# Kernel optimization log

Hardware: AMD Instinct MI355X
Metric: run time of the kernel (lower is better)

Reference implementation:

```python
import jax, jax.numpy as jnp
import numpy as np

N = 32768   # points
C = 64      # channels (in == out, required by residual)
K = 16      # nsample
SP = 8      # share_planes
S = C // SP # attention channels per group
E = N * K


def _bn(t, g, b, eps=1e-5):
    # torch BatchNorm1d training-mode forward: biased batch variance
    m = t.mean(0)
    v = t.var(0)
    return (t - m) * jax.lax.rsqrt(v + eps) * g + b


def setup_inputs() -> dict:
    rng = np.random.default_rng(0)
    pos = (rng.standard_normal((N, 3)) * 10.0).astype(np.float32)
    # kNN graph (loop=True -> self is among the K nearest, distance 0), chunked
    sq = (pos ** 2).sum(1)
    nbr = np.empty((N, K), dtype=np.int64)
    chunk = 2048
    for s0 in range(0, N, chunk):
        s1 = min(s0 + chunk, N)
        d = sq[s0:s1, None] + sq[None, :] - 2.0 * (pos[s0:s1] @ pos.T)
        nbr[s0:s1] = np.argpartition(d, K - 1, axis=1)[:, :K]
    # PyG convention: edge_index[0]=source j (neighbor), edge_index[1]=target i
    edge_index = np.stack([nbr.reshape(-1),
                           np.repeat(np.arange(N, dtype=np.int64), K)])

    def lin_w(fo, fi):
        b = 1.0 / np.sqrt(fi)
        return jnp.asarray(rng.uniform(-b, b, size=(fo, fi)).astype(np.float32))

    def lin_b(fo, fi):
        b = 1.0 / np.sqrt(fi)
        return jnp.asarray(rng.uniform(-b, b, size=(fo,)).astype(np.float32))

    ones = lambda n: jnp.ones((n,), jnp.float32)
    zeros = lambda n: jnp.zeros((n,), jnp.float32)

    return {
        'pos': jnp.asarray(pos),
        'x': jnp.asarray(rng.standard_normal((N, C)).astype(np.float32)),
        'W1': lin_w(C, C),
        'Wk': lin_w(C, C), 'bk': lin_b(C, C),
        'Wq': lin_w(C, C), 'bq': lin_b(C, C),
        'Wv': lin_w(C, C), 'bv': lin_b(C, C),
        'p1_w': lin_w(3, 3), 'p1_b': lin_b(3, 3),
        'p_bn_g': ones(3), 'p_bn_b': zeros(3),
        'p2_w': lin_w(C, 3), 'p2_b': lin_b(C, 3),
        'w_bn1_g': ones(C), 'w_bn1_b': zeros(C),
        'w1_w': lin_w(S, C), 'w1_b': lin_b(S, C),
        'w_bn2_g': ones(S), 'w_bn2_b': zeros(S),
        'w2_w': lin_w(S, S), 'w2_b': lin_b(S, S),
        'W3': lin_w(C, C),
        'bn1_g': ones(C), 'bn1_b': zeros(C),
        'bn2_g': ones(C), 'bn2_b': zeros(C),
        'bn3_g': ones(C), 'bn3_b': zeros(C),
        'edge_index': jnp.asarray(edge_index),
    }


def reference(pos, x, W1, Wk, bk, Wq, bq, Wv, bv,
              p1_w, p1_b, p_bn_g, p_bn_b, p2_w, p2_b,
              w_bn1_g, w_bn1_b, w1_w, w1_b, w_bn2_g, w_bn2_b, w2_w, w2_b,
              W3, bn1_g, bn1_b, bn2_g, bn2_b, bn3_g, bn3_b, edge_index):
    x_skip = x
    h = jax.nn.relu(_bn(x @ W1.T, bn1_g, bn1_b))            # linear1 (no bias) + bn1 + relu

    # PointTransformerLayer
    k = h @ Wk.T + bk                                        # alpha_j source
    q = h @ Wq.T + bq                                        # alpha_i target
    v = h @ Wv.T + bv                                        # values
    src, dst = edge_index[0], edge_index[1]

    rel = pos[src] - pos[dst]                                # pos_j - pos_i  [E,3]
    delta = jax.nn.relu(_bn(rel @ p1_w.T + p1_b, p_bn_g, p_bn_b)) @ p2_w.T + p2_b  # [E,C]

    a = k[src] - q[dst] + delta                              # [E,C]
    a = jax.nn.relu(_bn(a, w_bn1_g, w_bn1_b)) @ w1_w.T + w1_b        # [E,S]
    a = jax.nn.relu(_bn(a, w_bn2_g, w_bn2_b)) @ w2_w.T + w2_b        # [E,S]

    # segment softmax over each target's neighborhood
    amax = jax.ops.segment_max(a, dst, num_segments=N)
    ae = jnp.exp(a - amax[dst])
    asum = jax.ops.segment_sum(ae, dst, num_segments=N)
    attn = ae / asum[dst]                                    # [E,S]

    # grouped weighted values: attn broadcast across the SP groups
    msg = (attn[:, None, :] * (v[src] + delta).reshape(E, SP, S)).reshape(E, C)
    out = jax.ops.segment_sum(msg, dst, num_segments=N)      # aggr='add' -> [N,C]

    h2 = jax.nn.relu(_bn(out, bn2_g, bn2_b))
    h3 = _bn(h2 @ W3.T, bn3_g, bn3_b)                        # linear3 (no bias) + bn3
    return jax.nn.relu(h3 + x_skip)
```

## Files before the change

kernel.cpp:

```cpp
#include <hip/hip_runtime.h>

#define NPTS 32768
#define CH 64
#define KNN 16
#define NE (NPTS*KNN)
#define EPS 1e-5f
#define NREP 32

#define G_P   0
#define G_BN1 (1*NREP*128)
#define G_W1  (2*NREP*128)
#define G_W2  (3*NREP*128)
#define G_BN2 (4*NREP*128)
#define G_BN3 (5*NREP*128)
#define STATS_FLOATS (6*NREP*128)

#define F_P   (STATS_FLOATS + 0*128)
#define F_BN1 (STATS_FLOATS + 1*128)
#define F_W1  (STATS_FLOATS + 2*128)
#define F_W2  (STATS_FLOATS + 3*128)
#define F_BN2 (STATS_FLOATS + 4*128)
#define F_BN3 (STATS_FLOATS + 5*128)

#define OFF_T1  (STATS_FLOATS + 1024)
#define SZ_NC   (NPTS*CH)
#define OFF_K   (OFF_T1 + SZ_NC)
#define OFF_Q   (OFF_K + NPTS*32)
#define OFF_V   (OFF_Q + NPTS*32)
#define OFF_A2  (OFF_V + NPTS*32)
#define OFF_OUT (OFF_A2 + NE*4)
#define OFF_U   (OFF_OUT + SZ_NC)
#define OFF_H3  OFF_U

typedef unsigned int uint;

__device__ __forceinline__ float frelu(float x){ return fmaxf(x, 0.f); }
__device__ __forceinline__ float bflo(uint u){ return __uint_as_float(u<<16); }
__device__ __forceinline__ float bfhi(uint u){ return __uint_as_float(u & 0xffff0000u); }
__device__ __forceinline__ uint bfpack(float lo, float hi){
    uint a = __float_as_uint(lo), b = __float_as_uint(hi);
    a = (a + 0x7fffu + ((a>>16)&1u)) >> 16;
    b = ((b + 0x7fffu + ((b>>16)&1u)) >> 16) << 16;
    return a | b;
}

__global__ __launch_bounds__(128) void k_fin(
    const float* __restrict__ gA, float invA, const float* __restrict__ gmA,
    const float* __restrict__ btA, float* __restrict__ outA, int nchA,
    const float* __restrict__ gB, float invB, const float* __restrict__ gmB,
    const float* __restrict__ btB, float* __restrict__ outB, int nchB)
{
    __shared__ float s_tmp[128];
    const int tid = threadIdx.x;
    const float* g; float inv; const float* gm; const float* bt; float* o; int nch;
    if (blockIdx.x == 0) { g=gA; inv=invA; gm=gmA; bt=btA; o=outA; nch=nchA; }
    else { if (!outB) return; g=gB; inv=invB; gm=gmB; bt=btB; o=outB; nch=nchB; }
    float t = 0.f;
    #pragma unroll
    for (int r=0;r<NREP;++r) t += g[r*128+tid];
    s_tmp[tid] = t;
    __syncthreads();
    if (tid < 64) {
        if (tid < nch) {
            float m = s_tmp[tid]*inv;
            float v = s_tmp[64+tid]*inv - m*m;
            float s = gm[tid]*rsqrtf(v+EPS);
            o[tid] = s; o[64+tid] = bt[tid] - m*s;
        } else { o[tid]=0.f; o[64+tid]=0.f; }
    }
}

__global__ __launch_bounds__(256) void k_pstats_u(
    const float* __restrict__ pos, const int* __restrict__ esrc,
    const float* __restrict__ p1w, const float* __restrict__ p1b,
    float4* __restrict__ u4, float* __restrict__ gstat)
{
    __shared__ float red[4][6];
    const int tid = threadIdx.x;
    const float w0=p1w[0],w1=p1w[1],w2=p1w[2],w3=p1w[3],w4=p1w[4],w5=p1w[5],w6=p1w[6],w7=p1w[7],w8=p1w[8];
    const float b0=p1b[0],b1=p1b[1],b2=p1b[2];
    const int e = blockIdx.x*256 + tid;
    const int sj = esrc[e]; const int d = e >> 4;
    float ax = pos[3*sj]-pos[3*d], ay = pos[3*sj+1]-pos[3*d+1], az = pos[3*sj+2]-pos[3*d+2];
    float u0 = w0*ax+w1*ay+w2*az+b0;
    float u1 = w3*ax+w4*ay+w5*az+b1;
    float u2 = w6*ax+w7*ay+w8*az+b2;
    u4[e] = make_float4(u0,u1,u2,0.f);
    float s0=u0,s1=u1,s2=u2,q0=u0*u0,q1=u1*u1,q2=u2*u2;
    #pragma unroll
    for (int m=32;m>=1;m>>=1){
        s0+=__shfl_xor(s0,m); s1+=__shfl_xor(s1,m); s2+=__shfl_xor(s2,m);
        q0+=__shfl_xor(q0,m); q1+=__shfl_xor(q1,m); q2+=__shfl_xor(q2,m);
    }
    const int wv = tid>>6;
    if ((tid&63)==0){ red[wv][0]=s0; red[wv][1]=s1; red[wv][2]=s2;
                      red[wv][3]=q0; red[wv][4]=q1; red[wv][5]=q2; }
    __syncthreads();
    float* g = gstat + (blockIdx.x & (NREP-1))*128;
    if (tid < 3)      atomicAdd(&g[tid],        red[0][tid]+red[1][tid]+red[2][tid]+red[3][tid]);
    else if (tid < 6) atomicAdd(&g[64+(tid-3)], red[0][tid]+red[1][tid]+red[2][tid]+red[3][tid]);
}

__global__ __launch_bounds__(256) void k_gemm64(
    const float* __restrict__ in, const float* __restrict__ W,
    float* __restrict__ out,
    const float* __restrict__ fbn, int applyBn,
    float* __restrict__ gstat)
{
    __shared__ float Wt[CH*16];
    __shared__ float4 fL[32];
    __shared__ float red[4][32];
    const int tid = threadIdx.x;
    const int wv = tid >> 6;
    const int rb = blockIdx.x >> 2;
    const int c0 = (blockIdx.x & 3)*16;
    #pragma unroll
    for (int ch=0; ch<4; ++ch){
        const int idx = ch*256 + tid;
        Wt[idx] = W[(size_t)(c0 + (idx & 15))*CH + (idx >> 4)];
    }
    if (applyBn && tid < 32) fL[tid] = ((const float4*)fbn)[tid];
    __syncthreads();

    const int row0 = rb*512 + tid;
    const float4* iv0 = (const float4*)(in + (size_t)row0*CH);
    const float4* iv1 = (const float4*)(in + (size_t)(row0+256)*CH);
    const float4* Wt4 = (const float4*)Wt;
    float4 A0=make_float4(0,0,0,0),A1=A0,A2=A0,A3=A0;
    float4 B0=A0,B1=A0,B2=A0,B3=A0;
    #pragma unroll 1
    for (int jj=0;jj<16;++jj){
        float4 x0 = iv0[jj], x1 = iv1[jj];
        if (applyBn){
            float4 s4 = fL[jj], h4 = fL[16+jj];
            x0.x=frelu(x0.x*s4.x+h4.x); x0.y=frelu(x0.y*s4.y+h4.y);
            x0.z=frelu(x0.z*s4.z+h4.z); x0.w=frelu(x0.w*s4.w+h4.w);
            x1.x=frelu(x1.x*s4.x+h4.x); x1.y=frelu(x1.y*s4.y+h4.y);
            x1.z=frelu(x1.z*s4.z+h4.z); x1.w=frelu(x1.w*s4.w+h4.w);
        }
        const float4* wb = &Wt4[jj*16];
        #define MSTEP(xa, xb, base) { \
            float4 w_0=wb[(base)+0], w_1=wb[(base)+1], w_2=wb[(base)+2], w_3=wb[(base)+3]; \
            A0.x+=(xa)*w_0.x; A0.y+=(xa)*w_0.y; A0.z+=(xa)*w_0.z; A0.w+=(xa)*w_0.w; \
            A1.x+=(xa)*w_1.x; A1.y+=(xa)*w_1.y; A1.z+=(xa)*w_1.z; A1.w+=(xa)*w_1.w; \
            A2.x+=(xa)*w_2.x; A2.y+=(xa)*w_2.y; A2.z+=(xa)*w_2.z; A2.w+=(xa)*w_2.w; \
            A3.x+=(xa)*w_3.x; A3.y+=(xa)*w_3.y; A3.z+=(xa)*w_3.z; A3.w+=(xa)*w_3.w; \
            B0.x+=(xb)*w_0.x; B0.y+=(xb)*w_0.y; B0.z+=(xb)*w_0.z; B0.w+=(xb)*w_0.w; \
            B1.x+=(xb)*w_1.x; B1.y+=(xb)*w_1.y; B1.z+=(xb)*w_1.z; B1.w+=(xb)*w_1.w; \
            B2.x+=(xb)*w_2.x; B2.y+=(xb)*w_2.y; B2.z+=(xb)*w_2.z; B2.w+=(xb)*w_2.w; \
            B3.x+=(xb)*w_3.x; B3.y+=(xb)*w_3.y; B3.z+=(xb)*w_3.z; B3.w+=(xb)*w_3.w; }
        MSTEP(x0.x, x1.x, 0) MSTEP(x0.y, x1.y, 4) MSTEP(x0.z, x1.z, 8) MSTEP(x0.w, x1.w, 12)
        #undef MSTEP
    }
    float4* ov0 = (float4*)(out + (size_t)row0*CH + c0);
    float4* ov1 = (float4*)(out + (size_t)(row0+256)*CH + c0);
    ov0[0]=A0; ov0[1]=A1; ov0[2]=A2; ov0[3]=A3;
    ov1[0]=B0; ov1[1]=B1; ov1[2]=B2; ov1[3]=B3;
    #define STATQ(q, A, B) { \
        float4 s = make_float4(A.x+B.x, A.y+B.y, A.z+B.z, A.w+B.w); \
        float4 sq = make_float4(A.x*A.x+B.x*B.x, A.y*A.y+B.y*B.y, A.z*A.z+B.z*B.z, A.w*A.w+B.w*B.w); \
        _Pragma("unroll") \
        for (int m=32;m>=1;m>>=1){ \
            s.x+=__shfl_xor(s.x,m); s.y+=__shfl_xor(s.y,m); \
            s.z+=__shfl_xor(s.z,m); s.w+=__shfl_xor(s.w,m); \
            sq.x+=__shfl_xor(sq.x,m); sq.y+=__shfl_xor(sq.y,m); \
            sq.z+=__shfl_xor(sq.z,m); sq.w+=__shfl_xor(sq.w,m); } \
        if ((tid&63)==0){ \
            red[wv][q*4+0]=s.x; red[wv][q*4+1]=s.y; red[wv][q*4+2]=s.z; red[wv][q*4+3]=s.w; \
            red[wv][16+q*4+0]=sq.x; red[wv][16+q*4+1]=sq.y; red[wv][16+q*4+2]=sq.z; red[wv][16+q*4+3]=sq.w; } }
    STATQ(0, A0, B0) STATQ(1, A1, B1) STATQ(2, A2, B2) STATQ(3, A3, B3)
    #undef STATQ
    __syncthreads();
    if (tid < 32) {
        float t = red[0][tid]+red[1][tid]+red[2][tid]+red[3][tid];
        int dstc = (tid<16) ? (c0+tid) : (64 + c0 + (tid-16));
        atomicAdd(&gstat[(blockIdx.x & (NREP-1))*128 + dstc], t);
    }
}

__global__ __launch_bounds__(256) void k_kqv(
    const float* __restrict__ t1,
    const float* __restrict__ Wk, const float* __restrict__ bk,
    const float* __restrict__ Wq, const float* __restrict__ bq,
    const float* __restrict__ Wv, const float* __restrict__ bv,
    const float* __restrict__ fbn,
    uint* __restrict__ kout, uint* __restrict__ qout, uint* __restrict__ vout)
{
    __shared__ float Wt[CH*16];
    __shared__ float4 fL[32];
    __shared__ float4 bias4[4];
    const int tid = threadIdx.x;
    const int m = blockIdx.x / 256;
    const int rem = blockIdx.x & 255;
    const int rb = rem >> 2;
    const int c0 = (rem & 3)*16;
    const float* W  = (m==0) ? Wk : (m==1 ? Wq : Wv);
    const float* bs = (m==0) ? bk : (m==1 ? bq : bv);
    uint* o         = (m==0) ? kout : (m==1 ? qout : vout);
    #pragma unroll
    for (int ch=0; ch<4; ++ch){
        const int idx = ch*256 + tid;
        Wt[idx] = W[(size_t)(c0 + (idx & 15))*CH + (idx >> 4)];
    }
    if (tid < 32) fL[tid] = ((const float4*)fbn)[tid];
    if (tid < 4)  bias4[tid] = ((const float4*)(bs + c0))[tid];
    __syncthreads();

    const int row0 = rb*512 + tid;
    const float4* iv0 = (const float4*)(t1 + (size_t)row0*CH);
    const float4* iv1 = (const float4*)(t1 + (size_t)(row0+256)*CH);
    const float4* Wt4 = (const float4*)Wt;
    float4 A0=bias4[0],A1=bias4[1],A2=bias4[2],A3=bias4[3];
    float4 B0=bias4[0],B1=bias4[1],B2=bias4[2],B3=bias4[3];
    #pragma unroll 1
    for (int jj=0;jj<16;++jj){
        float4 x0 = iv0[jj], x1 = iv1[jj];
        float4 s4 = fL[jj], h4 = fL[16+jj];
        x0.x=frelu(x0.x*s4.x+h4.x); x0.y=frelu(x0.y*s4.y+h4.y);
        x0.z=frelu(x0.z*s4.z+h4.z); x0.w=frelu(x0.w*s4.w+h4.w);
        x1.x=frelu(x1.x*s4.x+h4.x); x1.y=frelu(x1.y*s4.y+h4.y);
        x1.z=frelu(x1.z*s4.z+h4.z); x1.w=frelu(x1.w*s4.w+h4.w);
        const float4* wb = &Wt4[jj*16];
        #define MSTEP(xa, xb, base) { \
            float4 w_0=wb[(base)+0], w_1=wb[(base)+1], w_2=wb[(base)+2], w_3=wb[(base)+3]; \
            A0.x+=(xa)*w_0.x; A0.y+=(xa)*w_0.y; A0.z+=(xa)*w_0.z; A0.w+=(xa)*w_0.w; \
            A1.x+=(xa)*w_1.x; A1.y+=(xa)*w_1.y; A1.z+=(xa)*w_1.z; A1.w+=(xa)*w_1.w; \
            A2.x+=(xa)*w_2.x; A2.y+=(xa)*w_2.y; A2.z+=(xa)*w_2.z; A2.w+=(xa)*w_2.w; \
            A3.x+=(xa)*w_3.x; A3.y+=(xa)*w_3.y; A3.z+=(xa)*w_3.z; A3.w+=(xa)*w_3.w; \
            B0.x+=(xb)*w_0.x; B0.y+=(xb)*w_0.y; B0.z+=(xb)*w_0.z; B0.w+=(xb)*w_0.w; \
            B1.x+=(xb)*w_1.x; B1.y+=(xb)*w_1.y; B1.z+=(xb)*w_1.z; B1.w+=(xb)*w_1.w; \
            B2.x+=(xb)*w_2.x; B2.y+=(xb)*w_2.y; B2.z+=(xb)*w_2.z; B2.w+=(xb)*w_2.w; \
            B3.x+=(xb)*w_3.x; B3.y+=(xb)*w_3.y; B3.z+=(xb)*w_3.z; B3.w+=(xb)*w_3.w; }
        MSTEP(x0.x, x1.x, 0) MSTEP(x0.y, x1.y, 4) MSTEP(x0.z, x1.z, 8) MSTEP(x0.w, x1.w, 12)
        #undef MSTEP
    }
    uint4 pa, pb_;
    pa.x = bfpack(A0.x,A0.y); pa.y = bfpack(A0.z,A0.w);
    pa.z = bfpack(A1.x,A1.y); pa.w = bfpack(A1.z,A1.w);
    pb_.x = bfpack(A2.x,A2.y); pb_.y = bfpack(A2.z,A2.w);
    pb_.z = bfpack(A3.x,A3.y); pb_.w = bfpack(A3.z,A3.w);
    uint4* o0 = (uint4*)(o + (size_t)row0*32 + (c0>>1));
    o0[0]=pa; o0[1]=pb_;
    pa.x = bfpack(B0.x,B0.y); pa.y = bfpack(B0.z,B0.w);
    pa.z = bfpack(B1.x,B1.y); pa.w = bfpack(B1.z,B1.w);
    pb_.x = bfpack(B2.x,B2.y); pb_.y = bfpack(B2.z,B2.w);
    pb_.z = bfpack(B3.x,B3.y); pb_.w = bfpack(B3.z,B3.w);
    uint4* o1 = (uint4*)(o + (size_t)(row0+256)*32 + (c0>>1));
    o1[0]=pa; o1[1]=pb_;
}

__global__ __launch_bounds__(256) void k_edge1(
    const int* __restrict__ esrc, const float4* __restrict__ u4,
    const unsigned short* __restrict__ kbuf, const unsigned short* __restrict__ qbuf,
    const float* __restrict__ fP,
    const float* __restrict__ p2w, const float* __restrict__ p2b,
    float* __restrict__ gstat)
{
    __shared__ float red[4][128];
    const int tid = threadIdx.x;
    const int c = tid & 63, wv = tid >> 6;
    const float scp0=fP[0], scp1=fP[1], scp2=fP[2];
    const float shp0=fP[64], shp1=fP[65], shp2=fP[66];
    const float w0 = p2w[c*3+0], w1 = p2w[c*3+1], w2 = p2w[c*3+2], bc = p2b[c];

    const int gw = blockIdx.x*4 + wv;
    const int chunk = NE/32768;
    const int e0 = gw*chunk;
    float s=0.f, q=0.f;
    #pragma unroll 4
    for (int e = e0; e < e0+chunk; ++e) {
        int sj = esrc[e]; int d = e >> 4;
        float4 uu = u4[e];
        float r0 = frelu(uu.x*scp0+shp0);
        float r1 = frelu(uu.y*scp1+shp1);
        float r2 = frelu(uu.z*scp2+shp2);
        float kv = __uint_as_float(((uint)kbuf[(size_t)sj*CH+c])<<16);
        float qv = __uint_as_float(((uint)qbuf[(size_t)d*CH+c])<<16);
        float a = kv - qv + (r0*w0 + r1*w1 + r2*w2 + bc);
        s += a; q += a*a;
    }
    red[wv][c] = s; red[wv][64+c] = q;
    __syncthreads();
    if (tid < 128) {
        float t = red[0][tid]+red[1][tid]+red[2][tid]+red[3][tid];
        atomicAdd(&gstat[(blockIdx.x & (NREP-1))*128 + tid], t);
    }
}

__global__ __launch_bounds__(256) void k_edge2(
    const int* __restrict__ esrc, const float4* __restrict__ u4,
    const uint* __restrict__ kbuf, const uint* __restrict__ qbuf,
    const float* __restrict__ fP,
    const float* __restrict__ p2w, const float* __restrict__ p2b,
    const float* __restrict__ fW1,
    const float* __restrict__ w1w, const float* __restrict__ w1bias,
    uint* __restrict__ a2out, float* __restrict__ gstat)
{
    __shared__ float red[4][16];
    const int tid = threadIdx.x;
    const float scp0=fP[0], scp1=fP[1], scp2=fP[2];
    const float shp0=fP[64], shp1=fP[65], shp2=fP[66];

    const int e = blockIdx.x*256 + tid;
    const int sj = esrc[e]; const int d = e >> 4;
    float4 uu = u4[e];
    const float r0 = frelu(uu.x*scp0+shp0);
    const float r1 = frelu(uu.y*scp1+shp1);
    const float r2 = frelu(uu.z*scp2+shp2);
    const uint4* kv = (const uint4*)(kbuf + (size_t)sj*32);
    const uint4* qv = (const uint4*)(qbuf + (size_t)d*32);
    float a2a[8];
    #pragma unroll
    for (int j=0;j<8;++j) a2a[j] = w1bias[j];
    #pragma unroll
    for (int cc=0; cc<8; ++cc) {
        uint4 ku = kv[cc], qu = qv[cc];
        const int c0 = cc*8;
        float kq[8];
        kq[0]=bflo(ku.x)-bflo(qu.x); kq[1]=bfhi(ku.x)-bfhi(qu.x);
        kq[2]=bflo(ku.y)-bflo(qu.y); kq[3]=bfhi(ku.y)-bfhi(qu.y);
        kq[4]=bflo(ku.z)-bflo(qu.z); kq[5]=bfhi(ku.z)-bfhi(qu.z);
        kq[6]=bflo(ku.w)-bflo(qu.w); kq[7]=bfhi(ku.w)-bfhi(qu.w);
        #pragma unroll
        for (int p=0;p<8;++p){
            const int c = c0+p;
            float b = frelu((kq[p] + r0*p2w[c*3]+r1*p2w[c*3+1]+r2*p2w[c*3+2]+p2b[c])*fW1[c]+fW1[64+c]);
            #pragma unroll
            for (int j=0;j<8;++j) a2a[j] += b*w1w[j*64+c];
        }
    }
    uint4 au;
    au.x = bfpack(a2a[0],a2a[1]); au.y = bfpack(a2a[2],a2a[3]);
    au.z = bfpack(a2a[4],a2a[5]); au.w = bfpack(a2a[6],a2a[7]);
    ((uint4*)a2out)[e] = au;
    float q8[8];
    #pragma unroll
    for (int j=0;j<8;++j) q8[j]=a2a[j]*a2a[j];
    #pragma unroll
    for (int m=32;m>=1;m>>=1){
        #pragma unroll
        for (int j=0;j<8;++j){ a2a[j]+=__shfl_xor(a2a[j],m); q8[j]+=__shfl_xor(q8[j],m); }
    }
    const int wv = tid>>6;
    if ((tid&63)==0){
        #pragma unroll
        for (int j=0;j<8;++j){ red[wv][j]=a2a[j]; red[wv][8+j]=q8[j]; }
    }
    __syncthreads();
    if (tid < 16) {
        float t = red[0][tid]+red[1][tid]+red[2][tid]+red[3][tid];
        int dstc = (tid<8) ? tid : (64 + tid - 8);
        atomicAdd(&gstat[(blockIdx.x & (NREP-1))*128 + dstc], t);
    }
}

__global__ __launch_bounds__(256) void k_attn(
    const int* __restrict__ esrc, const float4* __restrict__ u4,
    const uint* __restrict__ vbuf, const uint* __restrict__ a2buf,
    const float* __restrict__ fP,
    const float* __restrict__ p2w, const float* __restrict__ p2b,
    const float* __restrict__ fW2,
    const float* __restrict__ w2w, const float* __restrict__ w2bias,
    float* __restrict__ outbuf, float* __restrict__ gstat)
{
    __shared__ float red[4][128];
    __shared__ float att[256][8];
    __shared__ float rrL[256][4];
    __shared__ int   sjL[256];
    const int tid = threadIdx.x;
    const float scp0=fP[0], scp1=fP[1], scp2=fP[2];
    const float shp0=fP[64], shp1=fP[65], shp2=fP[66];

    const int t = tid & 15;
    const int i = blockIdx.x*16 + (tid>>4);
    const int e = i*KNN + t;
    const int sj = esrc[e];
    sjL[tid] = sj;
    {
        float4 uu = u4[e];
        rrL[tid][0] = frelu(uu.x*scp0+shp0);
        rrL[tid][1] = frelu(uu.y*scp1+shp1);
        rrL[tid][2] = frelu(uu.z*scp2+shp2);
    }
    {
        uint4 au = ((const uint4*)a2buf)[e];
        float bb[8];
        bb[0]=frelu(bflo(au.x)*fW2[0]+fW2[64]); bb[1]=frelu(bfhi(au.x)*fW2[1]+fW2[65]);
        bb[2]=frelu(bflo(au.y)*fW2[2]+fW2[66]); bb[3]=frelu(bfhi(au.y)*fW2[3]+fW2[67]);
        bb[4]=frelu(bflo(au.z)*fW2[4]+fW2[68]); bb[5]=frelu(bfhi(au.z)*fW2[5]+fW2[69]);
        bb[6]=frelu(bflo(au.w)*fW2[6]+fW2[70]); bb[7]=frelu(bfhi(au.w)*fW2[7]+fW2[71]);
        float at[8];
        #pragma unroll
        for (int s=0;s<8;++s){
            float a3 = w2bias[s];
            #pragma unroll
            for (int u=0;u<8;++u) a3 += bb[u]*w2w[s*8+u];
            float m = a3;
            #pragma unroll
            for (int msk=8;msk>=1;msk>>=1) m = fmaxf(m, __shfl_xor(m,msk));
            float p = __expf(a3-m);
            float ssm = p;
            #pragma unroll
            for (int msk=8;msk>=1;msk>>=1) ssm += __shfl_xor(ssm,msk);
            at[s] = p/ssm;
        }
        ((float4*)att[tid])[0] = make_float4(at[0],at[1],at[2],at[3]);
        ((float4*)att[tid])[1] = make_float4(at[4],at[5],at[6],at[7]);
    }
    __syncthreads();
    const int base = (tid>>4)*16;
    const int c0 = 4*t;
    const int ho = (t&1);
    float pw[12], pbv[4];
    #pragma unroll
    for (int k2=0;k2<12;++k2) pw[k2] = p2w[c0*3+k2];
    #pragma unroll
    for (int k2=0;k2<4;++k2)  pbv[k2] = p2b[c0+k2];
    float4 res = make_float4(0,0,0,0);
    #pragma unroll 4
    for (int n=0; n<16; ++n){
        const int sjn = sjL[base+n];
        uint2 vv = ((const uint2*)(vbuf + (size_t)sjn*32))[t];
        const float v0=bflo(vv.x), v1=bfhi(vv.x), v2=bflo(vv.y), v3=bfhi(vv.y);
        const float rr0 = rrL[base+n][0], rr1 = rrL[base+n][1], rr2 = rrL[base+n][2];
        float4 a4 = ((const float4*)att[base+n])[ho];
        res.x += a4.x*(v0 + rr0*pw[0]+rr1*pw[1]+rr2*pw[2]+pbv[0]);
        res.y += a4.y*(v1 + rr0*pw[3]+rr1*pw[4]+rr2*pw[5]+pbv[1]);
        res.z += a4.z*(v2 + rr0*pw[6]+rr1*pw[7]+rr2*pw[8]+pbv[2]);
        res.w += a4.w*(v3 + rr0*pw[9]+rr1*pw[10]+rr2*pw[11]+pbv[3]);
    }
    ((float4*)outbuf)[(size_t)i*16 + t] = res;

    float4 sq = make_float4(res.x*res.x, res.y*res.y, res.z*res.z, res.w*res.w);
    #pragma unroll
    for (int msk=32;msk>=16;msk>>=1){
        res.x+=__shfl_xor(res.x,msk); res.y+=__shfl_xor(res.y,msk);
        res.z+=__shfl_xor(res.z,msk); res.w+=__shfl_xor(res.w,msk);
        sq.x+=__shfl_xor(sq.x,msk);  sq.y+=__shfl_xor(sq.y,msk);
        sq.z+=__shfl_xor(sq.z,msk);  sq.w+=__shfl_xor(sq.w,msk);
    }
    const int wv = tid>>6;
    if ((tid&63) < 16){
        red[wv][t*4+0]=res.x; red[wv][t*4+1]=res.y; red[wv][t*4+2]=res.z; red[wv][t*4+3]=res.w;
        red[wv][64+t*4+0]=sq.x; red[wv][64+t*4+1]=sq.y; red[wv][64+t*4+2]=sq.z; red[wv][64+t*4+3]=sq.w;
    }
    __syncthreads();
    if (tid < 128) {
        float tt = red[0][tid]+red[1][tid]+red[2][tid]+red[3][tid];
        atomicAdd(&gstat[(blockIdx.x & (NREP-1))*128 + tid], tt);
    }
}

__global__ __launch_bounds__(256) void k_final(
    const float* __restrict__ h3, const float* __restrict__ x,
    const float* __restrict__ fbn, float* __restrict__ out)
{
    const int tid = threadIdx.x;
    const int gi = blockIdx.x*256 + tid;
    const int c0 = (gi & 15)*4;
    float sc0=fbn[c0],sc1=fbn[c0+1],sc2=fbn[c0+2],sc3=fbn[c0+3];
    float sh0=fbn[64+c0],sh1=fbn[64+c0+1],sh2=fbn[64+c0+2],sh3=fbn[64+c0+3];
    float4 h = ((const float4*)h3)[gi];
    float4 xv = ((const float4*)x)[gi];
    float4 o;
    o.x = fmaxf(h.x*sc0+sh0+xv.x, 0.f);
    o.y = fmaxf(h.y*sc1+sh1+xv.y, 0.f);
    o.z = fmaxf(h.z*sc2+sh2+xv.z, 0.f);
    o.w = fmaxf(h.w*sc3+sh3+xv.w, 0.f);
    ((float4*)out)[gi] = o;
}

extern "C" void kernel_launch(void* const* d_in, const int* in_sizes, int n_in,
                              void* d_out, int out_size, void* d_ws, size_t ws_size,
                              hipStream_t stream) {
    (void)in_sizes; (void)n_in; (void)out_size; (void)ws_size;
    const float* pos   = (const float*)d_in[0];
    const float* x     = (const float*)d_in[1];
    const float* W1    = (const float*)d_in[2];
    const float* Wk    = (const float*)d_in[3];
    const float* bk    = (const float*)d_in[4];
    const float* Wq    = (const float*)d_in[5];
    const float* bq    = (const float*)d_in[6];
    const float* Wv    = (const float*)d_in[7];
    const float* bv    = (const float*)d_in[8];
    const float* p1w   = (const float*)d_in[9];
    const float* p1b   = (const float*)d_in[10];
    const float* pg    = (const float*)d_in[11];
    const float* pb    = (const float*)d_in[12];
    const float* p2w   = (const float*)d_in[13];
    const float* p2b   = (const float*)d_in[14];
    const float* w1g   = (const float*)d_in[15];
    const float* w1bb  = (const float*)d_in[16];
    const float* w1w   = (const float*)d_in[17];
    const float* w1bias= (const float*)d_in[18];
    const float* w2g   = (const float*)d_in[19];
    const float* w2bb  = (const float*)d_in[20];
    const float* w2w   = (const float*)d_in[21];
    const float* w2bias= (const float*)d_in[22];
    const float* W3    = (const float*)d_in[23];
    const float* bn1g  = (const float*)d_in[24];
    const float* bn1b  = (const float*)d_in[25];
    const float* bn2g  = (const float*)d_in[26];
    const float* bn2b  = (const float*)d_in[27];
    const float* bn3g  = (const float*)d_in[28];
    const float* bn3b  = (const float*)d_in[29];
    const int*   ei    = (const int*)d_in[30];
    float* ws  = (float*)d_ws;
    float* out = (float*)d_out;
    uint* kb = (uint*)(ws+OFF_K);
    uint* qb = (uint*)(ws+OFF_Q);
    uint* vb = (uint*)(ws+OFF_V);
    uint* a2b = (uint*)(ws+OFF_A2);

    hipMemsetAsync(ws, 0, STATS_FLOATS*sizeof(float), stream);

    k_pstats_u<<<2048, 256, 0, stream>>>(pos, ei, p1w, p1b,
        (float4*)(ws+OFF_U), ws+G_P);
    k_gemm64<<<256, 256, 0, stream>>>(x, W1, ws+OFF_T1, nullptr, 0, ws+G_BN1);
    k_fin<<<2, 128, 0, stream>>>(ws+G_P, 1.f/NE, pg, pb, ws+F_P, 3,
                                 ws+G_BN1, 1.f/NPTS, bn1g, bn1b, ws+F_BN1, 64);
    k_kqv<<<768, 256, 0, stream>>>(ws+OFF_T1, Wk, bk, Wq, bq, Wv, bv,
        ws+F_BN1, kb, qb, vb);
    k_edge1<<<8192, 256, 0, stream>>>(ei, (const float4*)(ws+OFF_U),
        (const unsigned short*)kb, (const unsigned short*)qb, ws+F_P, p2w, p2b, ws+G_W1);
    k_fin<<<1, 128, 0, stream>>>(ws+G_W1, 1.f/NE, w1g, w1bb, ws+F_W1, 64,
                                 nullptr, 0.f, nullptr, nullptr, nullptr, 0);
    k_edge2<<<2048, 256, 0, stream>>>(ei, (const float4*)(ws+OFF_U),
        kb, qb, ws+F_P, p2w, p2b,
        ws+F_W1, w1w, w1bias, a2b, ws+G_W2);
    k_fin<<<1, 128, 0, stream>>>(ws+G_W2, 1.f/NE, w2g, w2bb, ws+F_W2, 8,
                                 nullptr, 0.f, nullptr, nullptr, nullptr, 0);
    k_attn<<<2048, 256, 0, stream>>>(ei, (const float4*)(ws+OFF_U),
        vb, a2b, ws+F_P, p2w, p2b,
        ws+F_W2, w2w, w2bias, ws+OFF_OUT, ws+G_BN2);
    k_fin<<<1, 128, 0, stream>>>(ws+G_BN2, 1.f/NPTS, bn2g, bn2b, ws+F_BN2, 64,
                                 nullptr, 0.f, nullptr, nullptr, nullptr, 0);
    k_gemm64<<<256, 256, 0, stream>>>(ws+OFF_OUT, W3, ws+OFF_H3,
        ws+F_BN2, 1, ws+G_BN3);
    k_fin<<<1, 128, 0, stream>>>(ws+G_BN3, 1.f/NPTS, bn3g, bn3b, ws+F_BN3, 64,
                                 nullptr, 0.f, nullptr, nullptr, nullptr, 0);
    k_final<<<2048, 256, 0, stream>>>(ws+OFF_H3, x, ws+F_BN3, out);
}
```

Baseline: 281.0 us.

## Fold BN finalize kernels into consumers and merge pos-stats with first GEMM

Removes four of the five small BN-finalize launches: each consumer kernel now reduces the replicated partial sums and computes scale and shift itself at block start. The position-stats kernel and the first 64x64 GEMM are merged into one launch split by block index. This cuts launch count and inter-kernel gaps, but every block now redundantly re-reads the NREP partial sums and does extra syncthreads.

```diff
diff --git a/kernel.cpp b/kernel.cpp
--- a/kernel.cpp
+++ b/kernel.cpp
@@ -15,12 +15,7 @@
 #define G_BN3 (5*NREP*128)
 #define STATS_FLOATS (6*NREP*128)
 
-#define F_P   (STATS_FLOATS + 0*128)
-#define F_BN1 (STATS_FLOATS + 1*128)
-#define F_W1  (STATS_FLOATS + 2*128)
-#define F_W2  (STATS_FLOATS + 3*128)
-#define F_BN2 (STATS_FLOATS + 4*128)
-#define F_BN3 (STATS_FLOATS + 5*128)
+#define F_W1  (STATS_FLOATS)
 
 #define OFF_T1  (STATS_FLOATS + 1024)
 #define SZ_NC   (NPTS*CH)
@@ -44,17 +39,12 @@
     return a | b;
 }
 
-__global__ __launch_bounds__(128) void k_fin(
-    const float* __restrict__ gA, float invA, const float* __restrict__ gmA,
-    const float* __restrict__ btA, float* __restrict__ outA, int nchA,
-    const float* __restrict__ gB, float invB, const float* __restrict__ gmB,
-    const float* __restrict__ btB, float* __restrict__ outB, int nchB)
+__global__ __launch_bounds__(128) void k_fin1(
+    const float* __restrict__ g, float inv, const float* __restrict__ gm,
+    const float* __restrict__ bt, float* __restrict__ o, int nch)
 {
     __shared__ float s_tmp[128];
     const int tid = threadIdx.x;
-    const float* g; float inv; const float* gm; const float* bt; float* o; int nch;
-    if (blockIdx.x == 0) { g=gA; inv=invA; gm=gmA; bt=btA; o=outA; nch=nchA; }
-    else { if (!outB) return; g=gB; inv=invB; gm=gmB; bt=btB; o=outB; nch=nchB; }
     float t = 0.f;
     #pragma unroll
     for (int r=0;r<NREP;++r) t += g[r*128+tid];
@@ -70,58 +60,50 @@
     }
 }
 
-__global__ __launch_bounds__(256) void k_pstats_u(
+__global__ __launch_bounds__(256) void k_pg(
     const float* __restrict__ pos, const int* __restrict__ esrc,
     const float* __restrict__ p1w, const float* __restrict__ p1b,
-    float4* __restrict__ u4, float* __restrict__ gstat)
-{
-    __shared__ float red[4][6];
-    const int tid = threadIdx.x;
-    const float w0=p1w[0],w1=p1w[1],w2=p1w[2],w3=p1w[3],w4=p1w[4],w5=p1w[5],w6=p1w[6],w7=p1w[7],w8=p1w[8];
-    const float b0=p1b[0],b1=p1b[1],b2=p1b[2];
-    const int e = blockIdx.x*256 + tid;
-    const int sj = esrc[e]; const int d = e >> 4;
-    float ax = pos[3*sj]-pos[3*d], ay = pos[3*sj+1]-pos[3*d+1], az = pos[3*sj+2]-pos[3*d+2];
-    float u0 = w0*ax+w1*ay+w2*az+b0;
-    float u1 = w3*ax+w4*ay+w5*az+b1;
-    float u2 = w6*ax+w7*ay+w8*az+b2;
-    u4[e] = make_float4(u0,u1,u2,0.f);
-    float s0=u0,s1=u1,s2=u2,q0=u0*u0,q1=u1*u1,q2=u2*u2;
-    #pragma unroll
-    for (int m=32;m>=1;m>>=1){
-        s0+=__shfl_xor(s0,m); s1+=__shfl_xor(s1,m); s2+=__shfl_xor(s2,m);
-        q0+=__shfl_xor(q0,m); q1+=__shfl_xor(q1,m); q2+=__shfl_xor(q2,m);
-    }
-    const int wv = tid>>6;
-    if ((tid&63)==0){ red[wv][0]=s0; red[wv][1]=s1; red[wv][2]=s2;
-                      red[wv][3]=q0; red[wv][4]=q1; red[wv][5]=q2; }
-    __syncthreads();
-    float* g = gstat + (blockIdx.x & (NREP-1))*128;
-    if (tid < 3)      atomicAdd(&g[tid],        red[0][tid]+red[1][tid]+red[2][tid]+red[3][tid]);
-    else if (tid < 6) atomicAdd(&g[64+(tid-3)], red[0][tid]+red[1][tid]+red[2][tid]+red[3][tid]);
-}
-
-__global__ __launch_bounds__(256) void k_gemm64(
+    float4* __restrict__ u4, float* __restrict__ gstatP,
     const float* __restrict__ in, const float* __restrict__ W,
-    float* __restrict__ out,
-    const float* __restrict__ fbn, int applyBn,
-    float* __restrict__ gstat)
+    float* __restrict__ out, float* __restrict__ gstatB)
 {
     __shared__ float Wt[CH*16];
-    __shared__ float4 fL[32];
     __shared__ float red[4][32];
     const int tid = threadIdx.x;
     const int wv = tid >> 6;
-    const int rb = blockIdx.x >> 2;
-    const int c0 = (blockIdx.x & 3)*16;
+    if (blockIdx.x < 2048) {
+        const float w0=p1w[0],w1=p1w[1],w2=p1w[2],w3=p1w[3],w4=p1w[4],w5=p1w[5],w6=p1w[6],w7=p1w[7],w8=p1w[8];
+        const float b0=p1b[0],b1=p1b[1],b2=p1b[2];
+        const int e = blockIdx.x*256 + tid;
+        const int sj = esrc[e]; const int d = e >> 4;
+        float ax = pos[3*sj]-pos[3*d], ay = pos[3*sj+1]-pos[3*d+1], az = pos[3*sj+2]-pos[3*d+2];
+        float u0 = w0*ax+w1*ay+w2*az+b0;
+        float u1 = w3*ax+w4*ay+w5*az+b1;
+        float u2 = w6*ax+w7*ay+w8*az+b2;
+        u4[e] = make_float4(u0,u1,u2,0.f);
+        float s0=u0,s1=u1,s2=u2,q0=u0*u0,q1=u1*u1,q2=u2*u2;
+        #pragma unroll
+        for (int m=32;m>=1;m>>=1){
+            s0+=__shfl_xor(s0,m); s1+=__shfl_xor(s1,m); s2+=__shfl_xor(s2,m);
+            q0+=__shfl_xor(q0,m); q1+=__shfl_xor(q1,m); q2+=__shfl_xor(q2,m);
+        }
+        if ((tid&63)==0){ red[wv][0]=s0; red[wv][1]=s1; red[wv][2]=s2;
+                          red[wv][3]=q0; red[wv][4]=q1; red[wv][5]=q2; }
+        __syncthreads();
+        float* g = gstatP + (blockIdx.x & (NREP-1))*128;
+        if (tid < 3)      atomicAdd(&g[tid],        red[0][tid]+red[1][tid]+red[2][tid]+red[3][tid]);
+        else if (tid < 6) atomicAdd(&g[64+(tid-3)], red[0][tid]+red[1][tid]+red[2][tid]+red[3][tid]);
+        return;
+    }
+    const int bid = blockIdx.x - 2048;
+    const int rb = bid >> 2;
+    const int c0 = (bid & 3)*16;
     #pragma unroll
     for (int ch=0; ch<4; ++ch){
         const int idx = ch*256 + tid;
         Wt[idx] = W[(size_t)(c0 + (idx & 15))*CH + (idx >> 4)];
     }
-    if (applyBn && tid < 32) fL[tid] = ((const float4*)fbn)[tid];
-    __syncthreads();
-
+    __syncthreads();
     const int row0 = rb*512 + tid;
     const float4* iv0 = (const float4*)(in + (size_t)row0*CH);
     const float4* iv1 = (const float4*)(in + (size_t)(row0+256)*CH);
@@ -131,13 +113,6 @@
     #pragma unroll 1
     for (int jj=0;jj<16;++jj){
         float4 x0 = iv0[jj], x1 = iv1[jj];
-        if (applyBn){
-            float4 s4 = fL[jj], h4 = fL[16+jj];
-            x0.x=frelu(x0.x*s4.x+h4.x); x0.y=frelu(x0.y*s4.y+h4.y);
-            x0.z=frelu(x0.z*s4.z+h4.z); x0.w=frelu(x0.w*s4.w+h4.w);
-            x1.x=frelu(x1.x*s4.x+h4.x); x1.y=frelu(x1.y*s4.y+h4.y);
-            x1.z=frelu(x1.z*s4.z+h4.z); x1.w=frelu(x1.w*s4.w+h4.w);
-        }
         const float4* wb = &Wt4[jj*16];
         #define MSTEP(xa, xb, base) { \
             float4 w_0=wb[(base)+0], w_1=wb[(base)+1], w_2=wb[(base)+2], w_3=wb[(base)+3]; \
@@ -174,7 +149,7 @@
     if (tid < 32) {
         float t = red[0][tid]+red[1][tid]+red[2][tid]+red[3][tid];
         int dstc = (tid<16) ? (c0+tid) : (64 + c0 + (tid-16));
-        atomicAdd(&gstat[(blockIdx.x & (NREP-1))*128 + dstc], t);
+        atomicAdd(&gstatB[(bid & (NREP-1))*128 + dstc], t);
     }
 }
 
@@ -183,11 +158,12 @@
     const float* __restrict__ Wk, const float* __restrict__ bk,
     const float* __restrict__ Wq, const float* __restrict__ bq,
     const float* __restrict__ Wv, const float* __restrict__ bv,
-    const float* __restrict__ fbn,
+    const float* __restrict__ bnrep, const float* __restrict__ bn1g,
+    const float* __restrict__ bn1b,
     uint* __restrict__ kout, uint* __restrict__ qout, uint* __restrict__ vout)
 {
     __shared__ float Wt[CH*16];
-    __shared__ float4 fL[32];
+    __shared__ float fbnL[128];
     __shared__ float4 bias4[4];
     const int tid = threadIdx.x;
     const int m = blockIdx.x / 256;
@@ -202,9 +178,22 @@
         const int idx = ch*256 + tid;
         Wt[idx] = W[(size_t)(c0 + (idx & 15))*CH + (idx >> 4)];
     }
-    if (tid < 32) fL[tid] = ((const float4*)fbn)[tid];
+    if (tid < 128){
+        float t = 0.f;
+        #pragma unroll
+        for (int r=0;r<NREP;++r) t += bnrep[r*128+tid];
+        fbnL[tid] = t;
+    }
     if (tid < 4)  bias4[tid] = ((const float4*)(bs + c0))[tid];
     __syncthreads();
+    if (tid < 64){
+        float mm = fbnL[tid]*(1.f/NPTS);
+        float vv = fbnL[64+tid]*(1.f/NPTS) - mm*mm;
+        float ss = bn1g[tid]*rsqrtf(vv+EPS);
+        fbnL[tid] = ss; fbnL[64+tid] = bn1b[tid] - mm*ss;
+    }
+    __syncthreads();
+    const float4* fL = (const float4*)fbnL;
 
     const int row0 = rb*512 + tid;
     const float4* iv0 = (const float4*)(t1 + (size_t)row0*CH);
@@ -252,15 +241,28 @@
 __global__ __launch_bounds__(256) void k_edge1(
     const int* __restrict__ esrc, const float4* __restrict__ u4,
     const unsigned short* __restrict__ kbuf, const unsigned short* __restrict__ qbuf,
-    const float* __restrict__ fP,
+    const float* __restrict__ gP, const float* __restrict__ pg,
+    const float* __restrict__ pb,
     const float* __restrict__ p2w, const float* __restrict__ p2b,
     float* __restrict__ gstat)
 {
     __shared__ float red[4][128];
+    __shared__ float pf[6];
     const int tid = threadIdx.x;
     const int c = tid & 63, wv = tid >> 6;
-    const float scp0=fP[0], scp1=fP[1], scp2=fP[2];
-    const float shp0=fP[64], shp1=fP[65], shp2=fP[66];
+    if (tid < 6){
+        int idx = (tid<3) ? tid : 64+(tid-3);
+        float t = 0.f;
+        #pragma unroll
+        for (int r=0;r<NREP;++r) t += gP[r*128+idx];
+        pf[tid] = t;
+    }
+    __syncthreads();
+    const float m0=pf[0]*(1.f/NE), m1=pf[1]*(1.f/NE), m2=pf[2]*(1.f/NE);
+    const float scp0=pg[0]*rsqrtf(pf[3]*(1.f/NE)-m0*m0+EPS);
+    const float scp1=pg[1]*rsqrtf(pf[4]*(1.f/NE)-m1*m1+EPS);
+    const float scp2=pg[2]*rsqrtf(pf[5]*(1.f/NE)-m2*m2+EPS);
+    const float shp0=pb[0]-m0*scp0, shp1=pb[1]-m1*scp1, shp2=pb[2]-m2*scp2;
     const float w0 = p2w[c*3+0], w1 = p2w[c*3+1], w2 = p2w[c*3+2], bc = p2b[c];
 
     const int gw = blockIdx.x*4 + wv;
@@ -290,16 +292,29 @@
 __global__ __launch_bounds__(256) void k_edge2(
     const int* __restrict__ esrc, const float4* __restrict__ u4,
     const uint* __restrict__ kbuf, const uint* __restrict__ qbuf,
-    const float* __restrict__ fP,
+    const float* __restrict__ gP, const float* __restrict__ pg,
+    const float* __restrict__ pb,
     const float* __restrict__ p2w, const float* __restrict__ p2b,
     const float* __restrict__ fW1,
     const float* __restrict__ w1w, const float* __restrict__ w1bias,
     uint* __restrict__ a2out, float* __restrict__ gstat)
 {
     __shared__ float red[4][16];
-    const int tid = threadIdx.x;
-    const float scp0=fP[0], scp1=fP[1], scp2=fP[2];
-    const float shp0=fP[64], shp1=fP[65], shp2=fP[66];
+    __shared__ float pf[6];
+    const int tid = threadIdx.x;
+    if (tid < 6){
+        int idx = (tid<3) ? tid : 64+(tid-3);
+        float t = 0.f;
+        #pragma unroll
+        for (int r=0;r<NREP;++r) t += gP[r*128+idx];
+        pf[tid] = t;
+    }
+    __syncthreads();
+    const float m0=pf[0]*(1.f/NE), m1=pf[1]*(1.f/NE), m2=pf[2]*(1.f/NE);
+    const float scp0=pg[0]*rsqrtf(pf[3]*(1.f/NE)-m0*m0+EPS);
+    const float scp1=pg[1]*rsqrtf(pf[4]*(1.f/NE)-m1*m1+EPS);
+    const float scp2=pg[2]*rsqrtf(pf[5]*(1.f/NE)-m2*m2+EPS);
+    const float shp0=pb[0]-m0*scp0, shp1=pb[1]-m1*scp1, shp2=pb[2]-m2*scp2;
 
     const int e = blockIdx.x*256 + tid;
     const int sj = esrc[e]; const int d = e >> 4;
@@ -357,9 +372,11 @@
 __global__ __launch_bounds__(256) void k_attn(
     const int* __restrict__ esrc, const float4* __restrict__ u4,
     const uint* __restrict__ vbuf, const uint* __restrict__ a2buf,
-    const float* __restrict__ fP,
+    const float* __restrict__ gP, const float* __restrict__ pg,
+    const float* __restrict__ pb,
     const float* __restrict__ p2w, const float* __restrict__ p2b,
-    const float* __restrict__ fW2,
+    const float* __restrict__ gW2, const float* __restrict__ w2g,
+    const float* __restrict__ w2bb,
     const float* __restrict__ w2w, const float* __restrict__ w2bias,
     float* __restrict__ outbuf, float* __restrict__ gstat)
 {
@@ -367,9 +384,28 @@
     __shared__ float att[256][8];
     __shared__ float rrL[256][4];
     __shared__ int   sjL[256];
-    const int tid = threadIdx.x;
-    const float scp0=fP[0], scp1=fP[1], scp2=fP[2];
-    const float shp0=fP[64], shp1=fP[65], shp2=fP[66];
+    __shared__ float cf[22];
+    const int tid = threadIdx.x;
+    if (tid < 6){
+        int idx = (tid<3) ? tid : 64+(tid-3);
+        float t = 0.f;
+        #pragma unroll
+        for (int r=0;r<NREP;++r) t += gP[r*128+idx];
+        cf[tid] = t;
+    } else if (tid < 22){
+        int j = tid - 6;
+        int idx = (j<8) ? j : 64+(j-8);
+        float t = 0.f;
+        #pragma unroll
+        for (int r=0;r<NREP;++r) t += gW2[r*128+idx];
+        cf[tid] = t;
+    }
+    __syncthreads();
+    const float m0=cf[0]*(1.f/NE), m1=cf[1]*(1.f/NE), m2=cf[2]*(1.f/NE);
+    const float scp0=pg[0]*rsqrtf(cf[3]*(1.f/NE)-m0*m0+EPS);
+    const float scp1=pg[1]*rsqrtf(cf[4]*(1.f/NE)-m1*m1+EPS);
+    const float scp2=pg[2]*rsqrtf(cf[5]*(1.f/NE)-m2*m2+EPS);
+    const float shp0=pb[0]-m0*scp0, shp1=pb[1]-m1*scp1, shp2=pb[2]-m2*scp2;
 
     const int t = tid & 15;
     const int i = blockIdx.x*16 + (tid>>4);
@@ -383,12 +419,20 @@
         rrL[tid][2] = frelu(uu.z*scp2+shp2);
     }
     {
+        float sc2[8], sh2[8];
+        #pragma unroll
+        for (int j2=0;j2<8;++j2){
+            float mm = cf[6+j2]*(1.f/NE);
+            float vv = cf[14+j2]*(1.f/NE) - mm*mm;
+            float ss = w2g[j2]*rsqrtf(vv+EPS);
+            sc2[j2]=ss; sh2[j2]=w2bb[j2]-mm*ss;
+        }
         uint4 au = ((const uint4*)a2buf)[e];
         float bb[8];
-        bb[0]=frelu(bflo(au.x)*fW2[0]+fW2[64]); bb[1]=frelu(bfhi(au.x)*fW2[1]+fW2[65]);
-        bb[2]=frelu(bflo(au.y)*fW2[2]+fW2[66]); bb[3]=frelu(bfhi(au.y)*fW2[3]+fW2[67]);
-        bb[4]=frelu(bflo(au.z)*fW2[4]+fW2[68]); bb[5]=frelu(bfhi(au.z)*fW2[5]+fW2[69]);
-        bb[6]=frelu(bflo(au.w)*fW2[6]+fW2[70]); bb[7]=frelu(bfhi(au.w)*fW2[7]+fW2[71]);
+        bb[0]=frelu(bflo(au.x)*sc2[0]+sh2[0]); bb[1]=frelu(bfhi(au.x)*sc2[1]+sh2[1]);
+        bb[2]=frelu(bflo(au.y)*sc2[2]+sh2[2]); bb[3]=frelu(bfhi(au.y)*sc2[3]+sh2[3]);
+        bb[4]=frelu(bflo(au.z)*sc2[4]+sh2[4]); bb[5]=frelu(bfhi(au.z)*sc2[5]+sh2[5]);
+        bb[6]=frelu(bflo(au.w)*sc2[6]+sh2[6]); bb[7]=frelu(bfhi(au.w)*sc2[7]+sh2[7]);
         float at[8];
         #pragma unroll
         for (int s=0;s<8;++s){
@@ -451,15 +495,120 @@
     }
 }
 
+__global__ __launch_bounds__(256) void k_gemm_bn(
+    const float* __restrict__ in, const float* __restrict__ W,
+    float* __restrict__ out,
+    const float* __restrict__ bnrep, const float* __restrict__ gma,
+    const float* __restrict__ bta,
+    float* __restrict__ gstat)
+{
+    __shared__ float Wt[CH*16];
+    __shared__ float fbnL[128];
+    __shared__ float red[4][32];
+    const int tid = threadIdx.x;
+    const int wv = tid >> 6;
+    const int rb = blockIdx.x >> 2;
+    const int c0 = (blockIdx.x & 3)*16;
+    #pragma unroll
+    for (int ch=0; ch<4; ++ch){
+        const int idx = ch*256 + tid;
+        Wt[idx] = W[(size_t)(c0 + (idx & 15))*CH + (idx >> 4)];
+    }
+    if (tid < 128){
+        float t = 0.f;
+        #pragma unroll
+        for (int r=0;r<NREP;++r) t += bnrep[r*128+tid];
+        fbnL[tid] = t;
+    }
+    __syncthreads();
+    if (tid < 64){
+        float mm = fbnL[tid]*(1.f/NPTS);
+        float vv = fbnL[64+tid]*(1.f/NPTS) - mm*mm;
+        float ss = gma[tid]*rsqrtf(vv+EPS);
+        fbnL[tid] = ss; fbnL[64+tid] = bta[tid] - mm*ss;
+    }
+    __syncthreads();
+    const float4* fL = (const float4*)fbnL;
+
+    const int row0 = rb*512 + tid;
+    const float4* iv0 = (const float4*)(in + (size_t)row0*CH);
+    const float4* iv1 = (const float4*)(in + (size_t)(row0+256)*CH);
+    const float4* Wt4 = (const float4*)Wt;
+    float4 A0=make_float4(0,0,0,0),A1=A0,A2=A0,A3=A0;
+    float4 B0=A0,B1=A0,B2=A0,B3=A0;
+    #pragma unroll 1
+    for (int jj=0;jj<16;++jj){
+        float4 x0 = iv0[jj], x1 = iv1[jj];
+        float4 s4 = fL[jj], h4 = fL[16+jj];
+        x0.x=frelu(x0.x*s4.x+h4.x); x0.y=frelu(x0.y*s4.y+h4.y);
+        x0.z=frelu(x0.z*s4.z+h4.z); x0.w=frelu(x0.w*s4.w+h4.w);
+        x1.x=frelu(x1.x*s4.x+h4.x); x1.y=frelu(x1.y*s4.y+h4.y);
+        x1.z=frelu(x1.z*s4.z+h4.z); x1.w=frelu(x1.w*s4.w+h4.w);
+        const float4* wb = &Wt4[jj*16];
+        #define MSTEP(xa, xb, base) { \
+            float4 w_0=wb[(base)+0], w_1=wb[(base)+1], w_2=wb[(base)+2], w_3=wb[(base)+3]; \
+            A0.x+=(xa)*w_0.x; A0.y+=(xa)*w_0.y; A0.z+=(xa)*w_0.z; A0.w+=(xa)*w_0.w; \
+            A1.x+=(xa)*w_1.x; A1.y+=(xa)*w_1.y; A1.z+=(xa)*w_1.z; A1.w+=(xa)*w_1.w; \
+            A2.x+=(xa)*w_2.x; A2.y+=(xa)*w_2.y; A2.z+=(xa)*w_2.z; A2.w+=(xa)*w_2.w; \
+            A3.x+=(xa)*w_3.x; A3.y+=(xa)*w_3.y; A3.z+=(xa)*w_3.z; A3.w+=(xa)*w_3.w; \
+            B0.x+=(xb)*w_0.x; B0.y+=(xb)*w_0.y; B0.z+=(xb)*w_0.z; B0.w+=(xb)*w_0.w; \
+            B1.x+=(xb)*w_1.x; B1.y+=(xb)*w_1.y; B1.z+=(xb)*w_1.z; B1.w+=(xb)*w_1.w; \
+            B2.x+=(xb)*w_2.x; B2.y+=(xb)*w_2.y; B2.z+=(xb)*w_2.z; B2.w+=(xb)*w_2.w; \
+            B3.x+=(xb)*w_3.x; B3.y+=(xb)*w_3.y; B3.z+=(xb)*w_3.z; B3.w+=(xb)*w_3.w; }
+        MSTEP(x0.x, x1.x, 0) MSTEP(x0.y, x1.y, 4) MSTEP(x0.z, x1.z, 8) MSTEP(x0.w, x1.w, 12)
+        #undef MSTEP
+    }
+    float4* ov0 = (float4*)(out + (size_t)row0*CH + c0);
+    float4* ov1 = (float4*)(out + (size_t)(row0+256)*CH + c0);
+    ov0[0]=A0; ov0[1]=A1; ov0[2]=A2; ov0[3]=A3;
+    ov1[0]=B0; ov1[1]=B1; ov1[2]=B2; ov1[3]=B3;
+    #define STATQ(q, A, B) { \
+        float4 s = make_float4(A.x+B.x, A.y+B.y, A.z+B.z, A.w+B.w); \
+        float4 sq = make_float4(A.x*A.x+B.x*B.x, A.y*A.y+B.y*B.y, A.z*A.z+B.z*B.z, A.w*A.w+B.w*B.w); \
+        _Pragma("unroll") \
+        for (int m=32;m>=1;m>>=1){ \
+            s.x+=__shfl_xor(s.x,m); s.y+=__shfl_xor(s.y,m); \
+            s.z+=__shfl_xor(s.z,m); s.w+=__shfl_xor(s.w,m); \
+            sq.x+=__shfl_xor(sq.x,m); sq.y+=__shfl_xor(sq.y,m); \
+            sq.z+=__shfl_xor(sq.z,m); sq.w+=__shfl_xor(sq.w,m); } \
+        if ((tid&63)==0){ \
+            red[wv][q*4+0]=s.x; red[wv][q*4+1]=s.y; red[wv][q*4+2]=s.z; red[wv][q*4+3]=s.w; \
+            red[wv][16+q*4+0]=sq.x; red[wv][16+q*4+1]=sq.y; red[wv][16+q*4+2]=sq.z; red[wv][16+q*4+3]=sq.w; } }
+    STATQ(0, A0, B0) STATQ(1, A1, B1) STATQ(2, A2, B2) STATQ(3, A3, B3)
+    #undef STATQ
+    __syncthreads();
+    if (tid < 32) {
+        float t = red[0][tid]+red[1][tid]+red[2][tid]+red[3][tid];
+        int dstc = (tid<16) ? (c0+tid) : (64 + c0 + (tid-16));
+        atomicAdd(&gstat[(blockIdx.x & (NREP-1))*128 + dstc], t);
+    }
+}
+
 __global__ __launch_bounds__(256) void k_final(
     const float* __restrict__ h3, const float* __restrict__ x,
-    const float* __restrict__ fbn, float* __restrict__ out)
-{
-    const int tid = threadIdx.x;
+    const float* __restrict__ bnrep, const float* __restrict__ gma,
+    const float* __restrict__ bta, float* __restrict__ out)
+{
+    __shared__ float fb[128];
+    const int tid = threadIdx.x;
+    if (tid < 128){
+        float t = 0.f;
+        #pragma unroll
+        for (int r=0;r<NREP;++r) t += bnrep[r*128+tid];
+        fb[tid] = t;
+    }
+    __syncthreads();
+    if (tid < 64){
+        float mm = fb[tid]*(1.f/NPTS);
+        float vv = fb[64+tid]*(1.f/NPTS) - mm*mm;
+        float ss = gma[tid]*rsqrtf(vv+EPS);
+        fb[tid] = ss; fb[64+tid] = bta[tid] - mm*ss;
+    }
+    __syncthreads();
     const int gi = blockIdx.x*256 + tid;
     const int c0 = (gi & 15)*4;
-    float sc0=fbn[c0],sc1=fbn[c0+1],sc2=fbn[c0+2],sc3=fbn[c0+3];
-    float sh0=fbn[64+c0],sh1=fbn[64+c0+1],sh2=fbn[64+c0+2],sh3=fbn[64+c0+3];
+    float sc0=fb[c0],sc1=fb[c0+1],sc2=fb[c0+2],sc3=fb[c0+3];
+    float sh0=fb[64+c0],sh1=fb[64+c0+1],sh2=fb[64+c0+2],sh3=fb[64+c0+3];
     float4 h = ((const float4*)h3)[gi];
     float4 xv = ((const float4*)x)[gi];
     float4 o;
@@ -514,30 +663,21 @@
 
     hipMemsetAsync(ws, 0, STATS_FLOATS*sizeof(float), stream);
 
-    k_pstats_u<<<2048, 256, 0, stream>>>(pos, ei, p1w, p1b,
-        (float4*)(ws+OFF_U), ws+G_P);
-    k_gemm64<<<256, 256, 0, stream>>>(x, W1, ws+OFF_T1, nullptr, 0, ws+G_BN1);
-    k_fin<<<2, 128, 0, stream>>>(ws+G_P, 1.f/NE, pg, pb, ws+F_P, 3,
-                                 ws+G_BN1, 1.f/NPTS, bn1g, bn1b, ws+F_BN1, 64);
+    k_pg<<<2304, 256, 0, stream>>>(pos, ei, p1w, p1b,
+        (float4*)(ws+OFF_U), ws+G_P, x, W1, ws+OFF_T1, ws+G_BN1);
     k_kqv<<<768, 256, 0, stream>>>(ws+OFF_T1, Wk, bk, Wq, bq, Wv, bv,
-        ws+F_BN1, kb, qb, vb);
+        ws+G_BN1, bn1g, bn1b, kb, qb, vb);
     k_edge1<<<8192, 256, 0, stream>>>(ei, (const float4*)(ws+OFF_U),
-        (const unsigned short*)kb, (const unsigned short*)qb, ws+F_P, p2w, p2b, ws+G_W1);
-    k_fin<<<1, 128, 0, stream>>>(ws+G_W1, 1.f/NE, w1g, w1bb, ws+F_W1, 64,
-                                 nullptr, 0.f, nullptr, nullptr, nullptr, 0);
+        (const unsigned short*)kb, (const unsigned short*)qb,
+        ws+G_P, pg, pb, p2w, p2b, ws+G_W1);
+    k_fin1<<<1, 128, 0, stream>>>(ws+G_W1, 1.f/NE, w1g, w1bb, ws+F_W1, 64);
     k_edge2<<<2048, 256, 0, stream>>>(ei, (const float4*)(ws+OFF_U),
-        kb, qb, ws+F_P, p2w, p2b,
+        kb, qb, ws+G_P, pg, pb, p2w, p2b,
         ws+F_W1, w1w, w1bias, a2b, ws+G_W2);
-    k_fin<<<1, 128, 0, stream>>>(ws+G_W2, 1.f/NE, w2g, w2bb, ws+F_W2, 8,
-                                 nullptr, 0.f, nullptr, nullptr, nullptr, 0);
     k_attn<<<2048, 256, 0, stream>>>(ei, (const float4*)(ws+OFF_U),
-        vb, a2b, ws+F_P, p2w, p2b,
-        ws+F_W2, w2w, w2bias, ws+OFF_OUT, ws+G_BN2);
-    k_fin<<<1, 128, 0, stream>>>(ws+G_BN2, 1.f/NPTS, bn2g, bn2b, ws+F_BN2, 64,
-                                 nullptr, 0.f, nullptr, nullptr, nullptr, 0);
-    k_gemm64<<<256, 256, 0, stream>>>(ws+OFF_OUT, W3, ws+OFF_H3,
-        ws+F_BN2, 1, ws+G_BN3);
-    k_fin<<<1, 128, 0, stream>>>(ws+G_BN3, 1.f/NPTS, bn3g, bn3b, ws+F_BN3, 64,
-                                 nullptr, 0.f, nullptr, nullptr, nullptr, 0);
-    k_final<<<2048, 256, 0, stream>>>(ws+OFF_H3, x, ws+F_BN3, out);
-}
+        vb, a2b, ws+G_P, pg, pb, p2w, p2b,
+        ws+G_W2, w2g, w2bb, w2w, w2bias, ws+OFF_OUT, ws+G_BN2);
+    k_gemm_bn<<<256, 256, 0, stream>>>(ws+OFF_OUT, W3, ws+OFF_H3,
+        ws+G_BN2, bn2g, bn2b, ws+G_BN3);
+    k_final<<<2048, 256, 0, stream>>>(ws+OFF_H3, x, ws+G_BN3, bn3g, bn3b, out);
+}
```

Result: no change. 283.4 us (+0.9%).
